# Optimization experiments

Measured on AMD Instinct MI355X. Metric: run time of the kernel, lower is better.

## Reference

```python
import jax, jax.numpy as jnp
import numpy as np

N_NODES = 100000
N_EDGES = 3200000
FEAT = 32
N_ITER = 6  # -> n_iter - 1 = 5 SimpleConv layers
MIN_VAL, MAX_VAL = 0.0, 2.0


def setup_inputs() -> dict:
    key = jax.random.key(0)
    k = jax.random.split(key, 6)
    return {
        "x": jax.random.uniform(k[0], (N_NODES, FEAT), dtype=jnp.float32) * 2.0,
        "edge_index": jax.random.randint(k[1], (2, N_EDGES), 0, N_NODES, dtype=jnp.int32),
        "edge_mask": jax.random.randint(k[2], (N_EDGES,), 0, 2, dtype=jnp.int32),
        "edge_scale": jax.random.uniform(k[3], (N_EDGES,), dtype=jnp.float32),
        "pert_mask": jax.random.uniform(k[4], (N_EDGES,), dtype=jnp.float32),
        "edge_weight": jax.random.uniform(k[5], (N_EDGES,), dtype=jnp.float32),
    }


def reference(x, edge_index, edge_mask, edge_scale, pert_mask, edge_weight):
    # edge_index *= edge_mask (masked edges collapse to node 0, as in the torch code)
    ei = edge_index * edge_mask.astype(edge_index.dtype)  # [2, E]
    src, dst = ei[0], ei[1]
    # edge_weight = (edge_weight * (1 - pert_mask) + pert_mask) * edge_scale
    w = (edge_weight * (1.0 - pert_mask) + pert_mask) * edge_scale  # [E]

    def step(x, _):
        # SimpleConv(aggr='sum'): out[dst] += w_e * x[src]
        msgs = x[src] * w[:, None]                                   # [E, F]
        x_new = jax.ops.segment_sum(msgs, dst, num_segments=N_NODES)  # [N, F]
        # max_update: x + Hardtanh(-1,1)(x_new - x)
        x_new = x + jnp.clip(x_new - x, -1.0, 1.0)
        # act: Hardtanh(min_val, max_val)
        return jnp.clip(x_new, MIN_VAL, MAX_VAL), None

    x, _ = jax.lax.scan(step, x, None, length=N_ITER - 1)
    return x
```

## Files before the change

kernel.cpp:

```cpp
#include <hip/hip_runtime.h>
#include <hip/hip_fp16.h>

#define NNODES 100000
#define NEDGES 3200000
#define FEAT 32
#define NITER 5
#define NF (NNODES * FEAT)

#define EDGE_BLOCKS (NEDGES / 256)

#define BUCK_SH 7
#define BUCK_SZ 128
#define NBK 782
#define CHUNKF 4096
#define NBF 782
#define NT (NBF * NBK)
#define NTB 598

__global__ void ws_kernel(const int* __restrict__ edge_index,
                          const int* __restrict__ edge_mask,
                          const float* __restrict__ edge_scale,
                          const float* __restrict__ pert_mask,
                          const float* __restrict__ edge_weight,
                          int* __restrict__ dstm,
                          int* __restrict__ wbuf,
                          float* __restrict__ S_part) {
    const int e = blockIdx.x * 256 + threadIdx.x;
    const int m = edge_mask[e];
    const float w = (edge_weight[e] * (1.0f - pert_mask[e]) + pert_mask[e]) * edge_scale[e];
    wbuf[e] = __float_as_int(w);
    dstm[e] = m ? edge_index[NEDGES + e] : -1;
    float ms = m ? 0.0f : w;
    __shared__ float s[256];
    s[threadIdx.x] = ms;
    __syncthreads();
    for (int off = 128; off; off >>= 1) {
        if (threadIdx.x < off) s[threadIdx.x] += s[threadIdx.x + off];
        __syncthreads();
    }
    if (threadIdx.x == 0) S_part[blockIdx.x] = s[0];
}

__global__ void sreduce_kernel(const float* __restrict__ S_part, float* __restrict__ S) {
    __shared__ float s[1024];
    float a = 0.0f;
    for (int i = threadIdx.x; i < EDGE_BLOCKS; i += 1024) a += S_part[i];
    s[threadIdx.x] = a;
    __syncthreads();
    for (int off = 512; off; off >>= 1) {
        if (threadIdx.x < off) s[threadIdx.x] += s[threadIdx.x + off];
        __syncthreads();
    }
    if (threadIdx.x == 0) *S = s[0];
}

__global__ void histmat_kernel(const int* __restrict__ dstm, int* __restrict__ M) {
    __shared__ int h[NBK];
    const int b = blockIdx.x;
    for (int k = threadIdx.x; k < NBK; k += 256) h[k] = 0;
    __syncthreads();
    const int base = b * CHUNKF;
    for (int it = 0; it < CHUNKF / 256; ++it) {
        const int e = base + it * 256 + threadIdx.x;
        if (e < NEDGES) {
            const int d = dstm[e];
            if (d >= 0) atomicAdd(&h[d >> BUCK_SH], 1);
        }
    }
    __syncthreads();
    for (int k = threadIdx.x; k < NBK; k += 256) M[b * NBK + k] = h[k];
}

__global__ void tscan1_kernel(const int* __restrict__ M, int* __restrict__ tb) {
    __shared__ int s[1024];
    const int i = blockIdx.x * 1024 + threadIdx.x;
    int v = 0;
    if (i < NT) v = M[(i % NBF) * NBK + (i / NBF)];
    s[threadIdx.x] = v;
    __syncthreads();
    for (int off = 512; off; off >>= 1) {
        if (threadIdx.x < off) s[threadIdx.x] += s[threadIdx.x + off];
        __syncthreads();
    }
    if (threadIdx.x == 0) tb[blockIdx.x] = s[0];
}

__global__ void tscan2_kernel(const int* __restrict__ tb, int* __restrict__ tboff,
                              int* __restrict__ bucket_base) {
    __shared__ int s[1024];
    const int tid = threadIdx.x;
    int v = (tid < NTB) ? tb[tid] : 0;
    s[tid] = v;
    __syncthreads();
    for (int off = 1; off < 1024; off <<= 1) {
        int t = (tid >= off) ? s[tid - off] : 0;
        __syncthreads();
        s[tid] += t;
        __syncthreads();
    }
    if (tid < NTB) tboff[tid] = s[tid] - v;
    if (tid == 1023) bucket_base[NBK] = s[1023];
}

__global__ void tscan3_kernel(const int* __restrict__ M, const int* __restrict__ tboff,
                              int* __restrict__ scanT, int* __restrict__ bucket_base) {
    __shared__ int s[1024];
    const int tid = threadIdx.x;
    const int i = blockIdx.x * 1024 + tid;
    int v = 0;
    if (i < NT) v = M[(i % NBF) * NBK + (i / NBF)];
    s[tid] = v;
    __syncthreads();
    for (int off = 1; off < 1024; off <<= 1) {
        int t = (tid >= off) ? s[tid - off] : 0;
        __syncthreads();
        s[tid] += t;
        __syncthreads();
    }
    if (i < NT) {
        const int excl = tboff[blockIdx.x] + s[tid] - v;
        scanT[i] = excl;
        if (i % NBF == 0) bucket_base[i / NBF] = excl;
    }
}

__global__ void fill782_kernel(const int* __restrict__ edge_index,
                               const int* __restrict__ dstm,
                               const int* __restrict__ wbuf,
                               const int* __restrict__ scanT,
                               int2* __restrict__ e8tmp) {
    __shared__ int off[NBK];
    const int b = blockIdx.x;
    for (int k = threadIdx.x; k < NBK; k += 256) off[k] = scanT[k * NBF + b];
    __syncthreads();
    const int base = b * CHUNKF;
    for (int it = 0; it < CHUNKF / 256; ++it) {
        const int e = base + it * 256 + threadIdx.x;
        if (e < NEDGES) {
            const int d = dstm[e];
            if (d >= 0) {
                const int k = d >> BUCK_SH;
                const int dstl = d & (BUCK_SZ - 1);
                const int pos = atomicAdd(&off[k], 1);
                e8tmp[pos] = make_int2(edge_index[e] | (dstl << 20), wbuf[e]);
            }
        }
    }
}

__global__ void bsort_kernel(const int2* __restrict__ e8tmp,
                             const int* __restrict__ bucket_base,
                             int2* __restrict__ e8,
                             int* __restrict__ row_ptr) {
    __shared__ int h[BUCK_SZ];
    __shared__ int s[BUCK_SZ];
    __shared__ int woff[BUCK_SZ];
    const int k = blockIdx.x;
    const int tid = threadIdx.x;
    const int base0 = bucket_base[k];
    const int cnt = bucket_base[k + 1] - base0;
    if (tid < BUCK_SZ) h[tid] = 0;
    __syncthreads();
    for (int i = tid; i < cnt; i += 256) {
        const int dstl = e8tmp[base0 + i].x >> 20;
        atomicAdd(&h[dstl], 1);
    }
    __syncthreads();
    if (tid < BUCK_SZ) s[tid] = h[tid];
    __syncthreads();
    for (int off = 1; off < BUCK_SZ; off <<= 1) {
        int t = 0;
        if (tid < BUCK_SZ && tid >= off) t = s[tid - off];
        __syncthreads();
        if (tid < BUCK_SZ) s[tid] += t;
        __syncthreads();
    }
    if (tid < BUCK_SZ) {
        const int excl = s[tid] - h[tid];
        const int d = k * BUCK_SZ + tid;
        if (d < NNODES) row_ptr[d] = base0 + excl;
        woff[tid] = excl;
    }
    if (k == NBK - 1 && tid == 0) row_ptr[NNODES] = bucket_base[NBK];
    __syncthreads();
    for (int i = tid; i < cnt; i += 256) {
        const int2 v = e8tmp[base0 + i];
        const int dstl = v.x >> 20;
        const int src = v.x & 0xFFFFF;
        const int pos = atomicAdd(&woff[dstl], 1);
        e8[base0 + pos] = make_int2(src << 5, v.y);
    }
}

__global__ void cvt_kernel(const float* __restrict__ x, __half* __restrict__ xh) {
    const int i = blockIdx.x * 256 + threadIdx.x;
    const float4 v = reinterpret_cast<const float4*>(x)[i];
    const int node = i >> 3;
    const int q = i & 7;
    const int fh = q >> 2;
    const int part = q & 3;
    __half2 h01 = __floats2half2_rn(v.x, v.y);
    __half2 h23 = __floats2half2_rn(v.z, v.w);
    *reinterpret_cast<uint2*>((char*)xh + (size_t)fh * (NNODES * 32) + node * 32 + part * 8)
        = make_uint2(*(unsigned*)&h01, *(unsigned*)&h23);
}

__global__ void gather_kernel(const __half* __restrict__ xh,
                              const int* __restrict__ row_ptr,
                              const int2* __restrict__ e8,
                              const float* __restrict__ S,
                              float* __restrict__ out,
                              __half* __restrict__ outh) {
    const int bid = blockIdx.x;
    const int r = bid & 7;
    const int fh = r >> 2;
    const int blk = (bid >> 3) * 4 + (r & 3);
    if (blk >= 6250) return;
    const int lane = threadIdx.x & 63;
    const int wid = threadIdx.x >> 6;
    const int nq   = lane >> 4;
    const int slot = (lane >> 1) & 7;
    const int part = lane & 1;
    const int node = blk * 16 + wid * 4 + nq;
    const int beg = row_ptr[node];
    const int end = row_ptr[node + 1];
    const char* xhc = (const char*)xh + (size_t)fh * (NNODES * 32);

    float a0=0.f,a1=0.f,a2=0.f,a3=0.f,a4=0.f,a5=0.f,a6=0.f,a7=0.f;
    const int em1c = (end - 1 > beg) ? (end - 1) : beg;
    for (int i = beg + slot; __any(i < end); i += 8) {
        const bool valid = (i < end);
        const int2 sw = e8[valid ? i : em1c];
        const float w = valid ? __int_as_float(sw.y) : 0.0f;
        const uint4 hv = *reinterpret_cast<const uint4*>(
            xhc + (size_t)(unsigned)sw.x + (part << 4));
        float2 f;
        f = __half22float2(*(const __half2*)&hv.x); a0 = fmaf(w, f.x, a0); a1 = fmaf(w, f.y, a1);
        f = __half22float2(*(const __half2*)&hv.y); a2 = fmaf(w, f.x, a2); a3 = fmaf(w, f.y, a3);
        f = __half22float2(*(const __half2*)&hv.z); a4 = fmaf(w, f.x, a4); a5 = fmaf(w, f.y, a5);
        f = __half22float2(*(const __half2*)&hv.w); a6 = fmaf(w, f.x, a6); a7 = fmaf(w, f.y, a7);
    }
    #pragma unroll
    for (int off = 2; off <= 8; off <<= 1) {
        a0 += __shfl_xor(a0, off); a1 += __shfl_xor(a1, off);
        a2 += __shfl_xor(a2, off); a3 += __shfl_xor(a3, off);
        a4 += __shfl_xor(a4, off); a5 += __shfl_xor(a5, off);
        a6 += __shfl_xor(a6, off); a7 += __shfl_xor(a7, off);
    }
    if ((lane & 14) == 0) {
        const uint4 hx = *reinterpret_cast<const uint4*>(xhc + node * 32 + (part << 4));
        float2 f;
        f = __half22float2(*(const __half2*)&hx.x); const float x0f = f.x, x1f = f.y;
        f = __half22float2(*(const __half2*)&hx.y); const float x2f = f.x, x3f = f.y;
        f = __half22float2(*(const __half2*)&hx.z); const float x4f = f.x, x5f = f.y;
        f = __half22float2(*(const __half2*)&hx.w); const float x6f = f.x, x7f = f.y;
        if (node == 0) {
            const float S0 = *S;
            a0 = fmaf(S0, x0f, a0); a1 = fmaf(S0, x1f, a1);
            a2 = fmaf(S0, x2f, a2); a3 = fmaf(S0, x3f, a3);
            a4 = fmaf(S0, x4f, a4); a5 = fmaf(S0, x5f, a5);
            a6 = fmaf(S0, x6f, a6); a7 = fmaf(S0, x7f, a7);
        }
        const float r0 = fminf(fmaxf(x0f + fminf(fmaxf(a0 - x0f, -1.f), 1.f), 0.f), 2.f);
        const float r1 = fminf(fmaxf(x1f + fminf(fmaxf(a1 - x1f, -1.f), 1.f), 0.f), 2.f);
        const float r2 = fminf(fmaxf(x2f + fminf(fmaxf(a2 - x2f, -1.f), 1.f), 0.f), 2.f);
        const float r3 = fminf(fmaxf(x3f + fminf(fmaxf(a3 - x3f, -1.f), 1.f), 0.f), 2.f);
        const float r4 = fminf(fmaxf(x4f + fminf(fmaxf(a4 - x4f, -1.f), 1.f), 0.f), 2.f);
        const float r5 = fminf(fmaxf(x5f + fminf(fmaxf(a5 - x5f, -1.f), 1.f), 0.f), 2.f);
        const float r6 = fminf(fmaxf(x6f + fminf(fmaxf(a6 - x6f, -1.f), 1.f), 0.f), 2.f);
        const float r7 = fminf(fmaxf(x7f + fminf(fmaxf(a7 - x7f, -1.f), 1.f), 0.f), 2.f);
        __half2 h0 = __floats2half2_rn(r0, r1);
        __half2 h1 = __floats2half2_rn(r2, r3);
        __half2 h2 = __floats2half2_rn(r4, r5);
        __half2 h3 = __floats2half2_rn(r6, r7);
        uint4 hh;
        hh.x = *(unsigned*)&h0; hh.y = *(unsigned*)&h1;
        hh.z = *(unsigned*)&h2; hh.w = *(unsigned*)&h3;
        *reinterpret_cast<uint4*>((char*)outh + (size_t)fh * (NNODES * 32)
                                  + node * 32 + (part << 4)) = hh;
        if (out) {
            float* op = out + node * FEAT + (fh << 4) + (part << 3);
            *reinterpret_cast<float4*>(op)     = make_float4(r0, r1, r2, r3);
            *reinterpret_cast<float4*>(op + 4) = make_float4(r4, r5, r6, r7);
        }
    }
}

extern "C" void kernel_launch(void* const* d_in, const int* in_sizes, int n_in,
                              void* d_out, int out_size, void* d_ws, size_t ws_size,
                              hipStream_t stream) {
    const float* x0         = (const float*)d_in[0];
    const int*   edge_index = (const int*)d_in[1];
    const int*   edge_mask  = (const int*)d_in[2];
    const float* edge_scale = (const float*)d_in[3];
    const float* pert_mask  = (const float*)d_in[4];
    const float* edge_weight= (const float*)d_in[5];
    float* xout = (float*)d_out;

    char* ws = (char*)d_ws;
    float* S        = (float*)(ws);
    float* S_part   = (float*)(ws + 1024);
    int*   tb       = (int*)(ws + 64 * 1024);
    int*   tboff    = (int*)(ws + 68 * 1024);
    int*   bbase    = (int*)(ws + 72 * 1024);
    int*   row_ptr  = (int*)(ws + 80 * 1024);
    int*   M        = (int*)(ws + 1024 * 1024);
    int*   scanT    = (int*)(ws + 4  * 1024 * 1024);
    int2*  e8tmp    = (int2*)(ws + 17 * 1024 * 1024);
    int2*  e8       = (int2*)(ws + 30 * 1024 * 1024);
    int*   wbuf     = (int*)(ws + 43 * 1024 * 1024);
    int*   dstm     = (int*)(ws + 56 * 1024 * 1024);
    __half* xh0     = (__half*)(ws + 43 * 1024 * 1024);
    __half* xh1     = (__half*)(ws + 50 * 1024 * 1024);

    ws_kernel<<<EDGE_BLOCKS, 256, 0, stream>>>(edge_index, edge_mask, edge_scale,
                                               pert_mask, edge_weight, dstm, wbuf, S_part);
    sreduce_kernel<<<1, 1024, 0, stream>>>(S_part, S);
    histmat_kernel<<<NBF, 256, 0, stream>>>(dstm, M);
    tscan1_kernel<<<NTB, 1024, 0, stream>>>(M, tb);
    tscan2_kernel<<<1, 1024, 0, stream>>>(tb, tboff, bbase);
    tscan3_kernel<<<NTB, 1024, 0, stream>>>(M, tboff, scanT, bbase);
    fill782_kernel<<<NBF, 256, 0, stream>>>(edge_index, dstm, wbuf, scanT, e8tmp);
    bsort_kernel<<<NBK, 256, 0, stream>>>(e8tmp, bbase, e8, row_ptr);
    cvt_kernel<<<NF / 4 / 256, 256, 0, stream>>>(x0, xh0);

    const int gblocks = 12504;
    __half* xhb[2] = { xh0, xh1 };
    for (int it = 0; it < NITER; ++it) {
        gather_kernel<<<gblocks, 256, 0, stream>>>(xhb[it & 1], row_ptr, e8, S,
                                                   (it == NITER - 1) ? xout : nullptr,
                                                   xhb[(it + 1) & 1]);
    }
}
```

Baseline: 243.7 us.

## Pack edge payload early, widen buckets, and prefetch edges in gather loop

The preprocessing now packs src, local dst and weight into one int2 payload plus a 16-bit bucket id per edge. The fill kernel therefore reads one packed record instead of three separate arrays. Buckets double to 256 nodes, which halves the bucket count and the scan sizes. The gather loop software-prefetches the next edge record with nontemporal loads and issues the self-feature load early to hide latency. The risks are extra register pressure in the gather kernel and a different workspace layout, where xh buffers now alias the pay region.

```diff
diff --git a/kernel.cpp b/kernel.cpp
--- a/kernel.cpp
+++ b/kernel.cpp
@@ -9,27 +9,29 @@
 
 #define EDGE_BLOCKS (NEDGES / 256)
 
-#define BUCK_SH 7
-#define BUCK_SZ 128
-#define NBK 782
+#define BUCK_SH 8
+#define BUCK_SZ 256
+#define NBK 391
 #define CHUNKF 4096
 #define NBF 782
 #define NT (NBF * NBK)
-#define NTB 598
+#define NTB 299
 
 __global__ void ws_kernel(const int* __restrict__ edge_index,
                           const int* __restrict__ edge_mask,
                           const float* __restrict__ edge_scale,
                           const float* __restrict__ pert_mask,
                           const float* __restrict__ edge_weight,
-                          int* __restrict__ dstm,
-                          int* __restrict__ wbuf,
+                          int2* __restrict__ pay,
+                          unsigned short* __restrict__ bkt,
                           float* __restrict__ S_part) {
     const int e = blockIdx.x * 256 + threadIdx.x;
     const int m = edge_mask[e];
     const float w = (edge_weight[e] * (1.0f - pert_mask[e]) + pert_mask[e]) * edge_scale[e];
-    wbuf[e] = __float_as_int(w);
-    dstm[e] = m ? edge_index[NEDGES + e] : -1;
+    const int src = edge_index[e];
+    const int dst = edge_index[NEDGES + e];
+    pay[e] = make_int2(src | ((dst & (BUCK_SZ - 1)) << 20), __float_as_int(w));
+    bkt[e] = m ? (unsigned short)(dst >> BUCK_SH) : (unsigned short)0xFFFFu;
     float ms = m ? 0.0f : w;
     __shared__ float s[256];
     s[threadIdx.x] = ms;
@@ -54,7 +56,7 @@
     if (threadIdx.x == 0) *S = s[0];
 }
 
-__global__ void histmat_kernel(const int* __restrict__ dstm, int* __restrict__ M) {
+__global__ void histmat_kernel(const unsigned short* __restrict__ bkt, int* __restrict__ M) {
     __shared__ int h[NBK];
     const int b = blockIdx.x;
     for (int k = threadIdx.x; k < NBK; k += 256) h[k] = 0;
@@ -63,8 +65,8 @@
     for (int it = 0; it < CHUNKF / 256; ++it) {
         const int e = base + it * 256 + threadIdx.x;
         if (e < NEDGES) {
-            const int d = dstm[e];
-            if (d >= 0) atomicAdd(&h[d >> BUCK_SH], 1);
+            const unsigned short k = bkt[e];
+            if (k != 0xFFFFu) atomicAdd(&h[k], 1);
         }
     }
     __syncthreads();
@@ -87,19 +89,19 @@
 
 __global__ void tscan2_kernel(const int* __restrict__ tb, int* __restrict__ tboff,
                               int* __restrict__ bucket_base) {
-    __shared__ int s[1024];
+    __shared__ int s[512];
     const int tid = threadIdx.x;
     int v = (tid < NTB) ? tb[tid] : 0;
     s[tid] = v;
     __syncthreads();
-    for (int off = 1; off < 1024; off <<= 1) {
+    for (int off = 1; off < 512; off <<= 1) {
         int t = (tid >= off) ? s[tid - off] : 0;
         __syncthreads();
         s[tid] += t;
         __syncthreads();
     }
     if (tid < NTB) tboff[tid] = s[tid] - v;
-    if (tid == 1023) bucket_base[NBK] = s[1023];
+    if (tid == 511) bucket_base[NBK] = s[511];
 }
 
 __global__ void tscan3_kernel(const int* __restrict__ M, const int* __restrict__ tboff,
@@ -124,9 +126,8 @@
     }
 }
 
-__global__ void fill782_kernel(const int* __restrict__ edge_index,
-                               const int* __restrict__ dstm,
-                               const int* __restrict__ wbuf,
+__global__ void fill782_kernel(const int2* __restrict__ pay,
+                               const unsigned short* __restrict__ bkt,
                                const int* __restrict__ scanT,
                                int2* __restrict__ e8tmp) {
     __shared__ int off[NBK];
@@ -137,12 +138,10 @@
     for (int it = 0; it < CHUNKF / 256; ++it) {
         const int e = base + it * 256 + threadIdx.x;
         if (e < NEDGES) {
-            const int d = dstm[e];
-            if (d >= 0) {
-                const int k = d >> BUCK_SH;
-                const int dstl = d & (BUCK_SZ - 1);
+            const unsigned short k = bkt[e];
+            if (k != 0xFFFFu) {
                 const int pos = atomicAdd(&off[k], 1);
-                e8tmp[pos] = make_int2(edge_index[e] | (dstl << 20), wbuf[e]);
+                e8tmp[pos] = pay[e];
             }
         }
     }
@@ -159,23 +158,22 @@
     const int tid = threadIdx.x;
     const int base0 = bucket_base[k];
     const int cnt = bucket_base[k + 1] - base0;
-    if (tid < BUCK_SZ) h[tid] = 0;
+    h[tid] = 0;
     __syncthreads();
     for (int i = tid; i < cnt; i += 256) {
         const int dstl = e8tmp[base0 + i].x >> 20;
         atomicAdd(&h[dstl], 1);
     }
     __syncthreads();
-    if (tid < BUCK_SZ) s[tid] = h[tid];
+    s[tid] = h[tid];
     __syncthreads();
     for (int off = 1; off < BUCK_SZ; off <<= 1) {
-        int t = 0;
-        if (tid < BUCK_SZ && tid >= off) t = s[tid - off];
-        __syncthreads();
-        if (tid < BUCK_SZ) s[tid] += t;
-        __syncthreads();
-    }
-    if (tid < BUCK_SZ) {
+        int t = (tid >= off) ? s[tid - off] : 0;
+        __syncthreads();
+        s[tid] += t;
+        __syncthreads();
+    }
+    {
         const int excl = s[tid] - h[tid];
         const int d = k * BUCK_SZ + tid;
         if (d < NNODES) row_ptr[d] = base0 + excl;
@@ -226,19 +224,34 @@
     const int end = row_ptr[node + 1];
     const char* xhc = (const char*)xh + (size_t)fh * (NNODES * 32);
 
+    const uint4 hx = *reinterpret_cast<const uint4*>(xhc + node * 32 + (part << 4));
+
     float a0=0.f,a1=0.f,a2=0.f,a3=0.f,a4=0.f,a5=0.f,a6=0.f,a7=0.f;
     const int em1c = (end - 1 > beg) ? (end - 1) : beg;
-    for (int i = beg + slot; __any(i < end); i += 8) {
-        const bool valid = (i < end);
-        const int2 sw = e8[valid ? i : em1c];
-        const float w = valid ? __int_as_float(sw.y) : 0.0f;
+    int i = beg + slot;
+    bool valid = (i < end);
+    long long sw8 = __builtin_nontemporal_load(
+        reinterpret_cast<const long long*>(e8 + (valid ? i : em1c)));
+    while (__any(valid)) {
+        const int inext = i + 8;
+        const bool vnext = (inext < end);
+        const bool anext = __any(vnext);
+        long long swn8 = 0;
+        if (anext) {
+            swn8 = __builtin_nontemporal_load(
+                reinterpret_cast<const long long*>(e8 + (vnext ? inext : em1c)));
+        }
+        const int sx = (int)(sw8 & 0xFFFFFFFFll);
+        const float w = valid ? __int_as_float((int)(sw8 >> 32)) : 0.0f;
         const uint4 hv = *reinterpret_cast<const uint4*>(
-            xhc + (size_t)(unsigned)sw.x + (part << 4));
+            xhc + (size_t)(unsigned)sx + (part << 4));
         float2 f;
         f = __half22float2(*(const __half2*)&hv.x); a0 = fmaf(w, f.x, a0); a1 = fmaf(w, f.y, a1);
         f = __half22float2(*(const __half2*)&hv.y); a2 = fmaf(w, f.x, a2); a3 = fmaf(w, f.y, a3);
         f = __half22float2(*(const __half2*)&hv.z); a4 = fmaf(w, f.x, a4); a5 = fmaf(w, f.y, a5);
         f = __half22float2(*(const __half2*)&hv.w); a6 = fmaf(w, f.x, a6); a7 = fmaf(w, f.y, a7);
+        if (!anext) break;
+        i = inext; valid = vnext; sw8 = swn8;
     }
     #pragma unroll
     for (int off = 2; off <= 8; off <<= 1) {
@@ -248,7 +261,6 @@
         a6 += __shfl_xor(a6, off); a7 += __shfl_xor(a7, off);
     }
     if ((lane & 14) == 0) {
-        const uint4 hx = *reinterpret_cast<const uint4*>(xhc + node * 32 + (part << 4));
         float2 f;
         f = __half22float2(*(const __half2*)&hx.x); const float x0f = f.x, x1f = f.y;
         f = __half22float2(*(const __half2*)&hx.y); const float x2f = f.x, x3f = f.y;
@@ -304,23 +316,23 @@
     int*   tboff    = (int*)(ws + 68 * 1024);
     int*   bbase    = (int*)(ws + 72 * 1024);
     int*   row_ptr  = (int*)(ws + 80 * 1024);
-    int*   M        = (int*)(ws + 1024 * 1024);
-    int*   scanT    = (int*)(ws + 4  * 1024 * 1024);
-    int2*  e8tmp    = (int2*)(ws + 17 * 1024 * 1024);
-    int2*  e8       = (int2*)(ws + 30 * 1024 * 1024);
-    int*   wbuf     = (int*)(ws + 43 * 1024 * 1024);
-    int*   dstm     = (int*)(ws + 56 * 1024 * 1024);
-    __half* xh0     = (__half*)(ws + 43 * 1024 * 1024);
-    __half* xh1     = (__half*)(ws + 50 * 1024 * 1024);
+    int*   M        = (int*)(ws + 1  * 1024 * 1024);
+    int*   scanT    = (int*)(ws + 3  * 1024 * 1024);
+    int2*  e8tmp    = (int2*)(ws + 5  * 1024 * 1024);
+    int2*  e8       = (int2*)(ws + 18 * 1024 * 1024);
+    int2*  pay      = (int2*)(ws + 31 * 1024 * 1024);
+    unsigned short* bkt = (unsigned short*)(ws + 57 * 1024 * 1024);
+    __half* xh0     = (__half*)(ws + 31 * 1024 * 1024);
+    __half* xh1     = (__half*)(ws + 38 * 1024 * 1024);
 
     ws_kernel<<<EDGE_BLOCKS, 256, 0, stream>>>(edge_index, edge_mask, edge_scale,
-                                               pert_mask, edge_weight, dstm, wbuf, S_part);
+                                               pert_mask, edge_weight, pay, bkt, S_part);
     sreduce_kernel<<<1, 1024, 0, stream>>>(S_part, S);
-    histmat_kernel<<<NBF, 256, 0, stream>>>(dstm, M);
+    histmat_kernel<<<NBF, 256, 0, stream>>>(bkt, M);
     tscan1_kernel<<<NTB, 1024, 0, stream>>>(M, tb);
-    tscan2_kernel<<<1, 1024, 0, stream>>>(tb, tboff, bbase);
+    tscan2_kernel<<<1, 512, 0, stream>>>(tb, tboff, bbase);
     tscan3_kernel<<<NTB, 1024, 0, stream>>>(M, tboff, scanT, bbase);
-    fill782_kernel<<<NBF, 256, 0, stream>>>(edge_index, dstm, wbuf, scanT, e8tmp);
+    fill782_kernel<<<NBF, 256, 0, stream>>>(pay, bkt, scanT, e8tmp);
     bsort_kernel<<<NBK, 256, 0, stream>>>(e8tmp, bbase, e8, row_ptr);
     cvt_kernel<<<NF / 4 / 256, 256, 0, stream>>>(x0, xh0);
 
```

Measured after the change: 273.3 us. +12.1%, slower.
